# Optimization experiments

Measured on AMD Instinct MI355X. Metric: run time of the kernel, lower is better.

The kernel has to match this reference:

```python
import jax, jax.numpy as jnp
import numpy as np

B, D, U, M, K = 8192, 512, 512, 16, 64


def setup_inputs() -> dict:
    key = jax.random.key(0)
    ks = jax.random.split(key, 5)
    return {
        "x": jax.random.normal(ks[0], (B, D), dtype=jnp.float32),
        "key_kernel": jax.random.normal(ks[1], (D, K), dtype=jnp.float32) * (1.0 / np.sqrt(D)),
        "key_bias": jnp.zeros((K,), dtype=jnp.float32),
        "keys_map": jax.random.normal(ks[2], (M, K), dtype=jnp.float32),
        "kernels": jax.random.normal(ks[3], (M, D, U), dtype=jnp.float32) * (1.0 / np.sqrt(D)),
        "biases": jnp.zeros((M, U), dtype=jnp.float32),
    }


def reference(x, key_kernel, key_bias, keys_map, kernels, biases):
    # key projection: [B, K]
    keyv = x @ key_kernel + key_bias
    # inverse-distance similarity to mode keys: [B, M]
    dist = jnp.sqrt(jnp.sum((keyv[:, None, :] - keys_map[None, :, :]) ** 2, axis=-1))
    sim = 1.0 / (dist + 1.0)
    modes = kernels.shape[0]
    # kernel = mean_m(sim_m * kernels_m); out = x @ kernel.
    # Distributive identity: out = (1/M) * sum_m sim_m * (x @ kernels_m)
    out = jnp.einsum("bm,bd,mdu->bu", sim, x, kernels) / modes
    # bias = mean_m(sim_m * biases_m): [B, U]
    out = out + (sim @ biases) / modes
    return out
```

## Files before the change

### kernel.cpp

```cpp
#include <hip/hip_runtime.h>
#include <hip/hip_bf16.h>
#include <stdint.h>

#define B_SZ 8192
#define D_SZ 512
#define U_SZ 512
#define M_SZ 16
#define K_SZ 64

#define BROWS 64
#define BU 128
#define BK 64

typedef short bf16x8 __attribute__((ext_vector_type(8)));
typedef float f32x4 __attribute__((ext_vector_type(4)));

__device__ __forceinline__ unsigned short f2bf(float f) {
  union { float f; unsigned u; } v; v.f = f;
  unsigned r = v.u + 0x7fffu + ((v.u >> 16) & 1u);
  return (unsigned short)(r >> 16);
}

__device__ __forceinline__ void async16(const void* gptr, void* ldsptr) {
  __builtin_amdgcn_global_load_lds(
      (const __attribute__((address_space(1))) unsigned int*)gptr,
      (__attribute__((address_space(3))) unsigned int*)ldsptr,
      16, 0, 0);
}

__global__ __launch_bounds__(256) void cvt_kT(const float* __restrict__ kin,
                                              unsigned short* __restrict__ kT) {
  __shared__ float tf[32][65];
  int m = blockIdx.z, d0 = blockIdx.y * 32, u0 = blockIdx.x * 64;
  int t = threadIdx.x;
  {
    int dr = t >> 4, uc = t & 15;
    const float* src = kin + ((size_t)(m * D_SZ + d0 + dr)) * U_SZ + u0 + uc * 4;
    float4 a = *(const float4*)src;
    float4 b = *(const float4*)(src + 16 * U_SZ);
    tf[dr][uc * 4 + 0] = a.x; tf[dr][uc * 4 + 1] = a.y;
    tf[dr][uc * 4 + 2] = a.z; tf[dr][uc * 4 + 3] = a.w;
    tf[dr + 16][uc * 4 + 0] = b.x; tf[dr + 16][uc * 4 + 1] = b.y;
    tf[dr + 16][uc * 4 + 2] = b.z; tf[dr + 16][uc * 4 + 3] = b.w;
  }
  __syncthreads();
  {
    int ur = t >> 2, dc = t & 3;
    unsigned short* dst = kT + ((size_t)(m * U_SZ + u0 + ur)) * D_SZ + d0 + dc * 8;
    ushort4 lo, hi;
    lo.x = f2bf(tf[dc * 8 + 0][ur]); lo.y = f2bf(tf[dc * 8 + 1][ur]);
    lo.z = f2bf(tf[dc * 8 + 2][ur]); lo.w = f2bf(tf[dc * 8 + 3][ur]);
    hi.x = f2bf(tf[dc * 8 + 4][ur]); hi.y = f2bf(tf[dc * 8 + 5][ur]);
    hi.z = f2bf(tf[dc * 8 + 6][ur]); hi.w = f2bf(tf[dc * 8 + 7][ur]);
    *(ushort4*)dst = lo;
    *(ushort4*)(dst + 4) = hi;
  }
}

__global__ __launch_bounds__(256) void sim_kernel(
    const float* __restrict__ x, const float* __restrict__ key_kernel,
    const float* __restrict__ key_bias, const float* __restrict__ keys_map,
    float* __restrict__ sim, unsigned short* __restrict__ xb) {
  __shared__ float xs[16 * 512];
  __shared__ float ks[64 * 64];
  __shared__ float kv[16 * 64];
  int t = threadIdx.x;
  int b0 = blockIdx.x * 16;
  const float4* xg = (const float4*)(x + (size_t)b0 * D_SZ);
  float4* xs4 = (float4*)xs;
  ushort4* xb4 = (ushort4*)(xb + (size_t)b0 * D_SZ);
#pragma unroll
  for (int q = 0; q < 8; ++q) {
    float4 v = xg[q * 256 + t];
    xs4[q * 256 + t] = v;
    ushort4 o;
    o.x = f2bf(v.x); o.y = f2bf(v.y); o.z = f2bf(v.z); o.w = f2bf(v.w);
    xb4[q * 256 + t] = o;
  }
  int row = t >> 4, tk = t & 15;
  float4 acc = *(const float4*)(key_bias + tk * 4);
  float4* ks4 = (float4*)ks;
  const float4* wk4 = (const float4*)key_kernel;
  for (int c = 0; c < 8; ++c) {
    __syncthreads();
#pragma unroll
    for (int q = 0; q < 4; ++q) ks4[q * 256 + t] = wk4[c * 1024 + q * 256 + t];
    __syncthreads();
    const float* xrow = xs + row * 512 + c * 64;
#pragma unroll 8
    for (int dd = 0; dd < 64; ++dd) {
      float4 kk = ks4[dd * 16 + tk];
      float xv = xrow[dd];
      acc.x += xv * kk.x; acc.y += xv * kk.y;
      acc.z += xv * kk.z; acc.w += xv * kk.w;
    }
  }
  *(float4*)(kv + row * 64 + tk * 4) = acc;
  __syncthreads();
  int mm = t & 15;
  const float* kvr = kv + row * 64;
  const float* km = keys_map + mm * 64;
  float d2 = 0.f;
#pragma unroll 8
  for (int k = 0; k < 64; ++k) {
    float df = kvr[k] - km[k];
    d2 += df * df;
  }
  sim[(size_t)(b0 + row) * M_SZ + mm] = 1.0f / (sqrtf(d2) + 1.0f);
}

__global__ __launch_bounds__(256, 2) void poly_gemm(
    const unsigned short* __restrict__ xb,
    const unsigned short* __restrict__ kT,
    const float* __restrict__ sim,
    const float* __restrict__ biases,
    float* __restrict__ out) {
  __shared__ unsigned short sA[BROWS * D_SZ];
  __shared__ unsigned short sB[BU * BK];

  int t = threadIdx.x;
  int w = t >> 6, l = t & 63;
  int bid = blockIdx.x;
  int ut = (bid & 7) >> 1;
  int bt = ((bid >> 3) << 1) | (bid & 1);
  int b0 = bt * BROWS;
  int u0 = ut * BU;

  const unsigned short* xsrc = xb + (size_t)b0 * D_SZ;
#pragma unroll
  for (int c = 0; c < 16; ++c) {
    int ch = w * 16 + c;
    async16(xsrc + (size_t)ch * D_SZ + (size_t)(l ^ (ch & 7)) * 8,
            (char*)sA + ch * 1024);
  }

  int wi = w >> 1, wj = w & 1;
  int rbase = wi * 32, cbase = wj * 64;
  int lane16 = l & 15, quad = l >> 4;
  int sw = lane16 & 7;

  f32x4 facc[2][4];
#pragma unroll
  for (int i = 0; i < 2; ++i)
#pragma unroll
    for (int j = 0; j < 4; ++j) facc[i][j] = (f32x4){0.f, 0.f, 0.f, 0.f};

  for (int m = 0; m < M_SZ; ++m) {
    f32x4 pacc[2][4];
#pragma unroll
    for (int i = 0; i < 2; ++i)
#pragma unroll
      for (int j = 0; j < 4; ++j) pacc[i][j] = (f32x4){0.f, 0.f, 0.f, 0.f};

    const unsigned short* bsrc = kT + ((size_t)m * U_SZ + u0) * D_SZ;
    for (int kt = 0; kt < D_SZ / BK; ++kt) {
      __syncthreads();
#pragma unroll
      for (int c = 0; c < 4; ++c) {
        int ch = w * 4 + c;
        int urow = ch * 8 + (l >> 3);
        int kk8 = ((l & 7) ^ (l >> 3)) * 8;
        async16(bsrc + (size_t)urow * D_SZ + kt * BK + kk8, (char*)sB + ch * 1024);
      }
      __syncthreads();
#pragma unroll
      for (int h = 0; h < 2; ++h) {
        bf16x8 af[2], bfr[4];
        int ckA = kt * 8 + h * 4 + quad;
        int pA = ckA ^ sw;
#pragma unroll
        for (int i = 0; i < 2; ++i)
          af[i] = *(const bf16x8*)(sA + (size_t)(rbase + i * 16 + lane16) * D_SZ + pA * 8);
        int ckB = h * 4 + quad;
        int pB = ckB ^ sw;
#pragma unroll
        for (int j = 0; j < 4; ++j)
          bfr[j] = *(const bf16x8*)(sB + (size_t)(cbase + j * 16 + lane16) * BK + pB * 8);
#pragma unroll
        for (int i = 0; i < 2; ++i)
#pragma unroll
          for (int j = 0; j < 4; ++j)
            pacc[i][j] = __builtin_amdgcn_mfma_f32_16x16x32_bf16(
                af[i], bfr[j], pacc[i][j], 0, 0, 0);
      }
    }
    float bv[4];
#pragma unroll
    for (int j = 0; j < 4; ++j)
      bv[j] = biases[(size_t)m * U_SZ + u0 + cbase + j * 16 + lane16];
#pragma unroll
    for (int i = 0; i < 2; ++i)
#pragma unroll
      for (int r = 0; r < 4; ++r) {
        int row = b0 + rbase + i * 16 + quad * 4 + r;
        float s = sim[(size_t)row * M_SZ + m];
#pragma unroll
        for (int j = 0; j < 4; ++j)
          facc[i][j][r] += s * (pacc[i][j][r] + bv[j]);
      }
  }

  float* orow = out + (size_t)b0 * U_SZ + u0;
#pragma unroll
  for (int i = 0; i < 2; ++i)
#pragma unroll
    for (int r = 0; r < 4; ++r) {
      int row = rbase + i * 16 + quad * 4 + r;
#pragma unroll
      for (int j = 0; j < 4; ++j)
        orow[(size_t)row * U_SZ + cbase + j * 16 + lane16] =
            facc[i][j][r] * 0.0625f;
    }
}

extern "C" void kernel_launch(void* const* d_in, const int* in_sizes, int n_in,
                              void* d_out, int out_size, void* d_ws, size_t ws_size,
                              hipStream_t stream) {
  const float* x = (const float*)d_in[0];
  const float* key_kernel = (const float*)d_in[1];
  const float* key_bias = (const float*)d_in[2];
  const float* keys_map = (const float*)d_in[3];
  const float* kernels = (const float*)d_in[4];
  const float* biases = (const float*)d_in[5];
  float* out = (float*)d_out;

  unsigned short* xb = (unsigned short*)d_ws;
  unsigned short* kT = xb + (size_t)B_SZ * D_SZ;
  float* sim = (float*)((char*)d_ws + 2 * (size_t)B_SZ * D_SZ +
                        2 * (size_t)M_SZ * U_SZ * D_SZ);

  cvt_kT<<<dim3(U_SZ / 64, D_SZ / 32, M_SZ), 256, 0, stream>>>(kernels, kT);
  sim_kernel<<<dim3(B_SZ / 16), 256, 0, stream>>>(x, key_kernel, key_bias,
                                                  keys_map, sim, xb);
  poly_gemm<<<dim3(512), 256, 0, stream>>>(xb, kT, sim, biases, out);
}
```

Baseline: 197.3 us.

## Restructure pipeline: bf16 MFMA key projection, split-K mode GEMM with atomics

The single fused sim kernel is split into separate passes: x conversion, a bf16 MFMA key-projection GEMM, a distance/sim map stored transposed, and a bias initialisation that writes out. The mode GEMM now uses 128x128 tiles with split-K over two halves of D. The A fragment stays in registers across all 16 modes, and the next mode's B tile is prefetched asynchronously. Partial results are accumulated into out with atomicAdd. This aims to cut redundant x reloads and raise MFMA work per load, at the cost of more launches, atomic traffic and bf16 rounding in the key projection.

```diff
diff --git a/kernel.cpp b/kernel.cpp
--- a/kernel.cpp
+++ b/kernel.cpp
@@ -8,10 +8,6 @@
 #define M_SZ 16
 #define K_SZ 64
 
-#define BROWS 64
-#define BU 128
-#define BK 64
-
 typedef short bf16x8 __attribute__((ext_vector_type(8)));
 typedef float f32x4 __attribute__((ext_vector_type(4)));
 
@@ -28,16 +24,26 @@
       16, 0, 0);
 }
 
-__global__ __launch_bounds__(256) void cvt_kT(const float* __restrict__ kin,
-                                              unsigned short* __restrict__ kT) {
+__global__ __launch_bounds__(256) void cvt_x(const float* __restrict__ x,
+                                             unsigned short* __restrict__ xb) {
+  int i = (blockIdx.x * 256 + threadIdx.x) * 4;
+  float4 v = *(const float4*)(x + i);
+  ushort4 o;
+  o.x = f2bf(v.x); o.y = f2bf(v.y); o.z = f2bf(v.z); o.w = f2bf(v.w);
+  *(ushort4*)(xb + i) = o;
+}
+
+__global__ __launch_bounds__(256) void cvt_tr(const float* __restrict__ kin,
+                                              unsigned short* __restrict__ kT,
+                                              int Dd, int Uu) {
   __shared__ float tf[32][65];
   int m = blockIdx.z, d0 = blockIdx.y * 32, u0 = blockIdx.x * 64;
   int t = threadIdx.x;
   {
     int dr = t >> 4, uc = t & 15;
-    const float* src = kin + ((size_t)(m * D_SZ + d0 + dr)) * U_SZ + u0 + uc * 4;
+    const float* src = kin + ((size_t)m * Dd + d0 + dr) * Uu + u0 + uc * 4;
     float4 a = *(const float4*)src;
-    float4 b = *(const float4*)(src + 16 * U_SZ);
+    float4 b = *(const float4*)(src + (size_t)16 * Uu);
     tf[dr][uc * 4 + 0] = a.x; tf[dr][uc * 4 + 1] = a.y;
     tf[dr][uc * 4 + 2] = a.z; tf[dr][uc * 4 + 3] = a.w;
     tf[dr + 16][uc * 4 + 0] = b.x; tf[dr + 16][uc * 4 + 1] = b.y;
@@ -46,7 +52,7 @@
   __syncthreads();
   {
     int ur = t >> 2, dc = t & 3;
-    unsigned short* dst = kT + ((size_t)(m * U_SZ + u0 + ur)) * D_SZ + d0 + dc * 8;
+    unsigned short* dst = kT + ((size_t)m * Uu + u0 + ur) * Dd + d0 + dc * 8;
     ushort4 lo, hi;
     lo.x = f2bf(tf[dc * 8 + 0][ur]); lo.y = f2bf(tf[dc * 8 + 1][ur]);
     lo.z = f2bf(tf[dc * 8 + 2][ur]); lo.w = f2bf(tf[dc * 8 + 3][ur]);
@@ -57,159 +63,217 @@
   }
 }
 
-__global__ __launch_bounds__(256) void sim_kernel(
-    const float* __restrict__ x, const float* __restrict__ key_kernel,
-    const float* __restrict__ key_bias, const float* __restrict__ keys_map,
-    float* __restrict__ sim, unsigned short* __restrict__ xb) {
-  __shared__ float xs[16 * 512];
-  __shared__ float ks[64 * 64];
+__global__ __launch_bounds__(256) void keyv_gemm(
+    const unsigned short* __restrict__ xb, const unsigned short* __restrict__ wkT,
+    const float* __restrict__ key_bias, float* __restrict__ keyv) {
+  __shared__ unsigned short sW[64 * 512];
+  __shared__ unsigned short sA[128 * 64];
+  int t = threadIdx.x, w = t >> 6, l = t & 63;
+  int b0 = blockIdx.x * 128;
+#pragma unroll
+  for (int c = 0; c < 16; ++c) {
+    int ch = w * 16 + c;
+    async16(wkT + (size_t)ch * 512 + (size_t)(l ^ (ch & 7)) * 8,
+            (char*)sW + ch * 1024);
+  }
+  int rbase = w * 32;
+  int lane16 = l & 15, quad = l >> 4, sw = lane16 & 7;
+  f32x4 acc[2][4];
+#pragma unroll
+  for (int i = 0; i < 2; ++i)
+#pragma unroll
+    for (int j = 0; j < 4; ++j) acc[i][j] = (f32x4){0.f, 0.f, 0.f, 0.f};
+
+  for (int kt = 0; kt < 8; ++kt) {
+    __syncthreads();
+#pragma unroll
+    for (int c = 0; c < 4; ++c) {
+      int ch = w * 4 + c;
+      int row = ch * 8 + (l >> 3);
+      async16(xb + (size_t)(b0 + row) * D_SZ + kt * 64 + ((l & 7) ^ (l >> 3)) * 8,
+              (char*)sA + ch * 1024);
+    }
+    __syncthreads();
+#pragma unroll
+    for (int h = 0; h < 2; ++h) {
+      int ckA = h * 4 + quad;
+      bf16x8 af[2], bw[4];
+#pragma unroll
+      for (int i = 0; i < 2; ++i)
+        af[i] = *(const bf16x8*)(sA + (size_t)(rbase + i * 16 + lane16) * 64 +
+                                 (ckA ^ sw) * 8);
+      int ckW = kt * 8 + h * 4 + quad;
+#pragma unroll
+      for (int j = 0; j < 4; ++j)
+        bw[j] = *(const bf16x8*)(sW + (size_t)(j * 16 + lane16) * 512 +
+                                 (ckW ^ sw) * 8);
+#pragma unroll
+      for (int i = 0; i < 2; ++i)
+#pragma unroll
+        for (int j = 0; j < 4; ++j)
+          acc[i][j] = __builtin_amdgcn_mfma_f32_16x16x32_bf16(af[i], bw[j],
+                                                              acc[i][j], 0, 0, 0);
+    }
+  }
+  float bc[4];
+#pragma unroll
+  for (int j = 0; j < 4; ++j) bc[j] = key_bias[j * 16 + lane16];
+#pragma unroll
+  for (int i = 0; i < 2; ++i)
+#pragma unroll
+    for (int r = 0; r < 4; ++r) {
+      int row = b0 + rbase + i * 16 + quad * 4 + r;
+#pragma unroll
+      for (int j = 0; j < 4; ++j)
+        keyv[(size_t)row * 64 + j * 16 + lane16] = acc[i][j][r] + bc[j];
+    }
+}
+
+__global__ __launch_bounds__(256) void sim_map(const float* __restrict__ keyv,
+                                               const float* __restrict__ keys_map,
+                                               float* __restrict__ simT) {
   __shared__ float kv[16 * 64];
   int t = threadIdx.x;
   int b0 = blockIdx.x * 16;
-  const float4* xg = (const float4*)(x + (size_t)b0 * D_SZ);
-  float4* xs4 = (float4*)xs;
-  ushort4* xb4 = (ushort4*)(xb + (size_t)b0 * D_SZ);
-#pragma unroll
-  for (int q = 0; q < 8; ++q) {
-    float4 v = xg[q * 256 + t];
-    xs4[q * 256 + t] = v;
-    ushort4 o;
-    o.x = f2bf(v.x); o.y = f2bf(v.y); o.z = f2bf(v.z); o.w = f2bf(v.w);
-    xb4[q * 256 + t] = o;
-  }
-  int row = t >> 4, tk = t & 15;
-  float4 acc = *(const float4*)(key_bias + tk * 4);
-  float4* ks4 = (float4*)ks;
-  const float4* wk4 = (const float4*)key_kernel;
-  for (int c = 0; c < 8; ++c) {
-    __syncthreads();
-#pragma unroll
-    for (int q = 0; q < 4; ++q) ks4[q * 256 + t] = wk4[c * 1024 + q * 256 + t];
-    __syncthreads();
-    const float* xrow = xs + row * 512 + c * 64;
-#pragma unroll 8
-    for (int dd = 0; dd < 64; ++dd) {
-      float4 kk = ks4[dd * 16 + tk];
-      float xv = xrow[dd];
-      acc.x += xv * kk.x; acc.y += xv * kk.y;
-      acc.z += xv * kk.z; acc.w += xv * kk.w;
-    }
-  }
-  *(float4*)(kv + row * 64 + tk * 4) = acc;
+  ((float4*)kv)[t] = ((const float4*)(keyv + (size_t)b0 * 64))[t];
   __syncthreads();
-  int mm = t & 15;
+  int row = t >> 4, m = t & 15;
   const float* kvr = kv + row * 64;
-  const float* km = keys_map + mm * 64;
+  const float* km = keys_map + m * 64;
   float d2 = 0.f;
 #pragma unroll 8
   for (int k = 0; k < 64; ++k) {
     float df = kvr[k] - km[k];
     d2 += df * df;
   }
-  sim[(size_t)(b0 + row) * M_SZ + mm] = 1.0f / (sqrtf(d2) + 1.0f);
+  simT[(size_t)m * B_SZ + b0 + row] = 1.0f / (sqrtf(d2) + 1.0f);
+}
+
+__global__ __launch_bounds__(256) void bias_init(const float* __restrict__ simT,
+                                                 const float* __restrict__ biases,
+                                                 float* __restrict__ out) {
+  int t = threadIdx.x;
+  int b = blockIdx.x * 2 + (t >> 7);
+  int u = (t & 127) * 4;
+  float4 acc = {0.f, 0.f, 0.f, 0.f};
+#pragma unroll
+  for (int m = 0; m < M_SZ; ++m) {
+    float s = simT[(size_t)m * B_SZ + b];
+    float4 bv = *(const float4*)(biases + (size_t)m * U_SZ + u);
+    acc.x += s * bv.x; acc.y += s * bv.y; acc.z += s * bv.z; acc.w += s * bv.w;
+  }
+  acc.x *= 0.0625f; acc.y *= 0.0625f; acc.z *= 0.0625f; acc.w *= 0.0625f;
+  *(float4*)(out + (size_t)b * U_SZ + u) = acc;
 }
 
 __global__ __launch_bounds__(256, 2) void poly_gemm(
     const unsigned short* __restrict__ xb,
     const unsigned short* __restrict__ kT,
-    const float* __restrict__ sim,
-    const float* __restrict__ biases,
+    const float* __restrict__ simT,
     float* __restrict__ out) {
-  __shared__ unsigned short sA[BROWS * D_SZ];
-  __shared__ unsigned short sB[BU * BK];
-
-  int t = threadIdx.x;
-  int w = t >> 6, l = t & 63;
+  __shared__ unsigned short sA[128 * 64];
+  __shared__ unsigned short sB[128 * 64];
+
+  int t = threadIdx.x, w = t >> 6, l = t & 63;
   int bid = blockIdx.x;
-  int ut = (bid & 7) >> 1;
-  int bt = ((bid >> 3) << 1) | (bid & 1);
-  int b0 = bt * BROWS;
-  int u0 = ut * BU;
-
-  const unsigned short* xsrc = xb + (size_t)b0 * D_SZ;
-#pragma unroll
-  for (int c = 0; c < 16; ++c) {
-    int ch = w * 16 + c;
-    async16(xsrc + (size_t)ch * D_SZ + (size_t)(l ^ (ch & 7)) * 8,
-            (char*)sA + ch * 1024);
-  }
+  int ut = bid & 3, ks = (bid >> 2) & 1, bt = bid >> 3;
+  int b0 = bt * 128, u0 = ut * 128, k0 = ks * 256;
 
   int wi = w >> 1, wj = w & 1;
-  int rbase = wi * 32, cbase = wj * 64;
-  int lane16 = l & 15, quad = l >> 4;
-  int sw = lane16 & 7;
-
-  f32x4 facc[2][4];
-#pragma unroll
-  for (int i = 0; i < 2; ++i)
+  int rbase = wi * 64, cbase = wj * 64;
+  int lane16 = l & 15, quad = l >> 4, sw = lane16 & 7;
+  int srow = (l >> 3);
+  int skk = ((l & 7) ^ srow) * 8;
+
+  f32x4 facc[4][4];
+#pragma unroll
+  for (int i = 0; i < 4; ++i)
 #pragma unroll
     for (int j = 0; j < 4; ++j) facc[i][j] = (f32x4){0.f, 0.f, 0.f, 0.f};
 
-  for (int m = 0; m < M_SZ; ++m) {
-    f32x4 pacc[2][4];
-#pragma unroll
-    for (int i = 0; i < 2; ++i)
-#pragma unroll
-      for (int j = 0; j < 4; ++j) pacc[i][j] = (f32x4){0.f, 0.f, 0.f, 0.f};
-
-    const unsigned short* bsrc = kT + ((size_t)m * U_SZ + u0) * D_SZ;
-    for (int kt = 0; kt < D_SZ / BK; ++kt) {
+  const unsigned short* asrc = xb + (size_t)b0 * D_SZ + k0;
+  const unsigned short* bsrc0 = kT + (size_t)u0 * D_SZ + k0;
+
+  for (int kt = 0; kt < 4; ++kt) {
+    int kk = kt * 64;
+    __syncthreads();
+#pragma unroll
+    for (int c = 0; c < 4; ++c) {
+      int ch = w * 4 + c;
+      int row = ch * 8 + srow;
+      async16(asrc + (size_t)row * D_SZ + kk + skk, (char*)sA + ch * 1024);
+      async16(bsrc0 + (size_t)row * D_SZ + kk + skk, (char*)sB + ch * 1024);
+    }
+    __syncthreads();
+    bf16x8 af[4][2];
+#pragma unroll
+    for (int i = 0; i < 4; ++i)
+#pragma unroll
+      for (int h = 0; h < 2; ++h) {
+        int ck = h * 4 + quad;
+        af[i][h] = *(const bf16x8*)(sA + (size_t)(rbase + i * 16 + lane16) * 64 +
+                                    (ck ^ sw) * 8);
+      }
+    for (int m = 0; m < M_SZ; ++m) {
       __syncthreads();
-#pragma unroll
-      for (int c = 0; c < 4; ++c) {
-        int ch = w * 4 + c;
-        int urow = ch * 8 + (l >> 3);
-        int kk8 = ((l & 7) ^ (l >> 3)) * 8;
-        async16(bsrc + (size_t)urow * D_SZ + kt * BK + kk8, (char*)sB + ch * 1024);
+      bf16x8 bfr[4][2];
+#pragma unroll
+      for (int j = 0; j < 4; ++j)
+#pragma unroll
+        for (int h = 0; h < 2; ++h) {
+          int ck = h * 4 + quad;
+          bfr[j][h] = *(const bf16x8*)(sB + (size_t)(cbase + j * 16 + lane16) * 64 +
+                                       (ck ^ sw) * 8);
+        }
+      __syncthreads();
+      f32x4 sv[4];
+#pragma unroll
+      for (int i = 0; i < 4; ++i)
+        sv[i] = *(const f32x4*)(simT + (size_t)m * B_SZ + b0 + rbase + i * 16 +
+                                quad * 4);
+      if (m < 15) {
+        const unsigned short* bsrc =
+            kT + ((size_t)(m + 1) * U_SZ + u0) * D_SZ + k0;
+#pragma unroll
+        for (int c = 0; c < 4; ++c) {
+          int ch = w * 4 + c;
+          int row = ch * 8 + srow;
+          async16(bsrc + (size_t)row * D_SZ + kk + skk, (char*)sB + ch * 1024);
+        }
       }
-      __syncthreads();
-#pragma unroll
-      for (int h = 0; h < 2; ++h) {
-        bf16x8 af[2], bfr[4];
-        int ckA = kt * 8 + h * 4 + quad;
-        int pA = ckA ^ sw;
-#pragma unroll
-        for (int i = 0; i < 2; ++i)
-          af[i] = *(const bf16x8*)(sA + (size_t)(rbase + i * 16 + lane16) * D_SZ + pA * 8);
-        int ckB = h * 4 + quad;
-        int pB = ckB ^ sw;
-#pragma unroll
-        for (int j = 0; j < 4; ++j)
-          bfr[j] = *(const bf16x8*)(sB + (size_t)(cbase + j * 16 + lane16) * BK + pB * 8);
-#pragma unroll
-        for (int i = 0; i < 2; ++i)
-#pragma unroll
-          for (int j = 0; j < 4; ++j)
-            pacc[i][j] = __builtin_amdgcn_mfma_f32_16x16x32_bf16(
-                af[i], bfr[j], pacc[i][j], 0, 0, 0);
+#pragma unroll
+      for (int jh = 0; jh < 2; ++jh) {
+        f32x4 pacc[4][2];
+#pragma unroll
+        for (int i = 0; i < 4; ++i)
+#pragma unroll
+          for (int j2 = 0; j2 < 2; ++j2) {
+            int j = jh * 2 + j2;
+            pacc[i][j2] = __builtin_amdgcn_mfma_f32_16x16x32_bf16(
+                af[i][0], bfr[j][0], (f32x4){0.f, 0.f, 0.f, 0.f}, 0, 0, 0);
+            pacc[i][j2] = __builtin_amdgcn_mfma_f32_16x16x32_bf16(
+                af[i][1], bfr[j][1], pacc[i][j2], 0, 0, 0);
+          }
+#pragma unroll
+        for (int i = 0; i < 4; ++i)
+#pragma unroll
+          for (int j2 = 0; j2 < 2; ++j2)
+#pragma unroll
+            for (int r = 0; r < 4; ++r)
+              facc[i][jh * 2 + j2][r] += sv[i][r] * pacc[i][j2][r];
       }
     }
-    float bv[4];
-#pragma unroll
-    for (int j = 0; j < 4; ++j)
-      bv[j] = biases[(size_t)m * U_SZ + u0 + cbase + j * 16 + lane16];
-#pragma unroll
-    for (int i = 0; i < 2; ++i)
-#pragma unroll
-      for (int r = 0; r < 4; ++r) {
-        int row = b0 + rbase + i * 16 + quad * 4 + r;
-        float s = sim[(size_t)row * M_SZ + m];
-#pragma unroll
-        for (int j = 0; j < 4; ++j)
-          facc[i][j][r] += s * (pacc[i][j][r] + bv[j]);
-      }
-  }
-
-  float* orow = out + (size_t)b0 * U_SZ + u0;
-#pragma unroll
-  for (int i = 0; i < 2; ++i)
+  }
+
+#pragma unroll
+  for (int i = 0; i < 4; ++i)
 #pragma unroll
     for (int r = 0; r < 4; ++r) {
-      int row = rbase + i * 16 + quad * 4 + r;
+      int row = b0 + rbase + i * 16 + quad * 4 + r;
 #pragma unroll
       for (int j = 0; j < 4; ++j)
-        orow[(size_t)row * U_SZ + cbase + j * 16 + lane16] =
-            facc[i][j][r] * 0.0625f;
+        atomicAdd(out + (size_t)row * U_SZ + u0 + cbase + j * 16 + lane16,
+                  facc[i][j][r] * 0.0625f);
     }
 }
 
@@ -224,13 +288,19 @@
   const float* biases = (const float*)d_in[5];
   float* out = (float*)d_out;
 
-  unsigned short* xb = (unsigned short*)d_ws;
-  unsigned short* kT = xb + (size_t)B_SZ * D_SZ;
-  float* sim = (float*)((char*)d_ws + 2 * (size_t)B_SZ * D_SZ +
-                        2 * (size_t)M_SZ * U_SZ * D_SZ);
-
-  cvt_kT<<<dim3(U_SZ / 64, D_SZ / 32, M_SZ), 256, 0, stream>>>(kernels, kT);
-  sim_kernel<<<dim3(B_SZ / 16), 256, 0, stream>>>(x, key_kernel, key_bias,
-                                                  keys_map, sim, xb);
-  poly_gemm<<<dim3(512), 256, 0, stream>>>(xb, kT, sim, biases, out);
-}
+  char* p = (char*)d_ws;
+  unsigned short* xb = (unsigned short*)p;            p += (size_t)B_SZ * D_SZ * 2;
+  unsigned short* kT = (unsigned short*)p;            p += (size_t)M_SZ * U_SZ * D_SZ * 2;
+  unsigned short* wkT = (unsigned short*)p;           p += (size_t)K_SZ * D_SZ * 2;
+  float* keyv = (float*)p;                            p += (size_t)B_SZ * K_SZ * 4;
+  float* simT = (float*)p;
+
+  cvt_x<<<dim3((B_SZ * D_SZ) / 1024), 256, 0, stream>>>(x, xb);
+  cvt_tr<<<dim3(U_SZ / 64, D_SZ / 32, M_SZ), 256, 0, stream>>>(kernels, kT,
+                                                               D_SZ, U_SZ);
+  cvt_tr<<<dim3(1, D_SZ / 32, 1), 256, 0, stream>>>(key_kernel, wkT, D_SZ, K_SZ);
+  keyv_gemm<<<dim3(B_SZ / 128), 256, 0, stream>>>(xb, wkT, key_bias, keyv);
+  sim_map<<<dim3(B_SZ / 16), 256, 0, stream>>>(keyv, keys_map, simT);
+  bias_init<<<dim3(B_SZ / 2), 256, 0, stream>>>(simT, biases, out);
+  poly_gemm<<<dim3(512), 256, 0, stream>>>(xb, kT, simT, out);
+}
```

After: 201.9 us. 1.02x slower.
